# Kernel tuning notes

Measured on AMD Instinct MI355X. Metric: run time of the kernel, lower is better.

Reference implementation:

```python
import jax, jax.numpy as jnp
import numpy as np

N_NODES = 50000
N_EDGES = 800000
IN_DIM = 128
OUT_DIM = 64


def setup_inputs() -> dict:
    key = jax.random.key(0)
    k1, k2, k3, k4, k5 = jax.random.split(key, 5)
    x = jax.random.normal(k1, (N_NODES, IN_DIM), dtype=jnp.float32)
    # Glorot-uniform-ish init for the GCN weight (weight_variable_glorot)
    limit = np.sqrt(6.0 / (IN_DIM + OUT_DIM)).astype(np.float32)
    weight = jax.random.uniform(k2, (IN_DIM, OUT_DIM), dtype=jnp.float32,
                                minval=-limit, maxval=limit)
    adj_row = jax.random.randint(k3, (N_EDGES,), 0, N_NODES, dtype=jnp.int32)
    adj_col = jax.random.randint(k4, (N_EDGES,), 0, N_NODES, dtype=jnp.int32)
    adj_val = jax.random.uniform(k5, (N_EDGES,), dtype=jnp.float32)
    return {"x": x, "weight": weight, "adj_row": adj_row,
            "adj_col": adj_col, "adj_val": adj_val}


def reference(x, weight, adj_row, adj_col, adj_val):
    # x: [N, F_in], weight: [F_in, F_out]; dropout=0.0 (default) is identity.
    xw = jnp.matmul(x, weight)                      # [N, F_out] dense GEMM
    # spmm(adj, xw) with adj in COO: gather neighbor feats, scale, scatter-add
    msg = adj_val[:, None] * xw[adj_col]            # [E, F_out]
    agg = jax.ops.segment_sum(msg, adj_row, num_segments=x.shape[0])  # [N, F_out]
    return jax.nn.relu(agg)
```

## Files before the change

### kernel.cpp

```cpp
#include <hip/hip_runtime.h>

#define IN_DIM 128
#define OUT_DIM 64
#define PADK 136
#define RB 64
#define RBSH 6
#define CAPB 1280
#define AB2 128

typedef float f32x4 __attribute__((ext_vector_type(4)));
typedef short bf16x8 __attribute__((ext_vector_type(8)));

__device__ __forceinline__ unsigned short f2bf(float f) {
    unsigned u = __float_as_uint(f);
    return (unsigned short)((u + 0x7FFFu + ((u >> 16) & 1u)) >> 16);
}
__device__ __forceinline__ float bf2f(unsigned short h) {
    return __uint_as_float((unsigned)h << 16);
}

__device__ __forceinline__ void gemm_body(const float* __restrict__ x,
                                          const float* __restrict__ w,
                                          unsigned short* __restrict__ xwb,
                                          int N, int blk) {
    __shared__ unsigned short Ahi[64 * PADK];
    __shared__ unsigned short Alo[64 * PADK];
    __shared__ unsigned short Bhi[64 * PADK];
    __shared__ unsigned short Blo[64 * PADK];

    const int t = threadIdx.x;
    const int r0 = blk * 64;

    {
        const int c = t >> 2;
        const int kb = (t & 3) * 32;
        for (int k4 = 0; k4 < 32; k4 += 4) {
            ushort4 h, l;
            float v0 = w[(kb + k4 + 0) * OUT_DIM + c];
            float v1 = w[(kb + k4 + 1) * OUT_DIM + c];
            float v2 = w[(kb + k4 + 2) * OUT_DIM + c];
            float v3 = w[(kb + k4 + 3) * OUT_DIM + c];
            h.x = f2bf(v0); l.x = f2bf(v0 - bf2f(h.x));
            h.y = f2bf(v1); l.y = f2bf(v1 - bf2f(h.y));
            h.z = f2bf(v2); l.z = f2bf(v2 - bf2f(h.z));
            h.w = f2bf(v3); l.w = f2bf(v3 - bf2f(h.w));
            *(ushort4*)&Bhi[c * PADK + kb + k4] = h;
            *(ushort4*)&Blo[c * PADK + kb + k4] = l;
        }
    }
    {
        const float4* x4 = (const float4*)x;
        for (int i = 0; i < 8; ++i) {
            const int f = i * 256 + t;
            const int rr = f >> 5;
            const int kk = (f & 31) * 4;
            int row = r0 + rr; if (row >= N) row = N - 1;
            float4 v = x4[(size_t)row * (IN_DIM / 4) + (kk >> 2)];
            ushort4 h, l;
            h.x = f2bf(v.x); l.x = f2bf(v.x - bf2f(h.x));
            h.y = f2bf(v.y); l.y = f2bf(v.y - bf2f(h.y));
            h.z = f2bf(v.z); l.z = f2bf(v.z - bf2f(h.z));
            h.w = f2bf(v.w); l.w = f2bf(v.w - bf2f(h.w));
            *(ushort4*)&Ahi[rr * PADK + kk] = h;
            *(ushort4*)&Alo[rr * PADK + kk] = l;
        }
    }
    __syncthreads();

    const int lane = t & 63;
    const int wv = t >> 6;
    const int m = lane & 15;
    const int quad = lane >> 4;

    bf16x8 ahi[4], alo[4];
#pragma unroll
    for (int ks = 0; ks < 4; ++ks) {
        const int off = (wv * 16 + m) * PADK + ks * 32 + quad * 8;
        ahi[ks] = *(const bf16x8*)&Ahi[off];
        alo[ks] = *(const bf16x8*)&Alo[off];
    }
#pragma unroll
    for (int ct = 0; ct < 4; ++ct) {
        f32x4 acc = {0.f, 0.f, 0.f, 0.f};
#pragma unroll
        for (int ks = 0; ks < 4; ++ks) {
            const int off = (ct * 16 + m) * PADK + ks * 32 + quad * 8;
            bf16x8 bh = *(const bf16x8*)&Bhi[off];
            bf16x8 bl = *(const bf16x8*)&Blo[off];
            acc = __builtin_amdgcn_mfma_f32_16x16x32_bf16(alo[ks], bh, acc, 0, 0, 0);
            acc = __builtin_amdgcn_mfma_f32_16x16x32_bf16(ahi[ks], bl, acc, 0, 0, 0);
            acc = __builtin_amdgcn_mfma_f32_16x16x32_bf16(ahi[ks], bh, acc, 0, 0, 0);
        }
#pragma unroll
        for (int i = 0; i < 4; ++i) {
            const int row = r0 + wv * 16 + quad * 4 + i;
            if (row < N) xwb[(size_t)row * OUT_DIM + ct * 16 + m] = f2bf(acc[i]);
        }
    }
}

__global__ __launch_bounds__(256) void gemm_only(const float* __restrict__ x,
                                                 const float* __restrict__ w,
                                                 unsigned short* __restrict__ xwb,
                                                 int N) {
    gemm_body(x, w, xwb, N, blockIdx.x);
}

__global__ __launch_bounds__(256) void afill(
        const int* __restrict__ arow, const int* __restrict__ acol,
        const float* __restrict__ aval, int* __restrict__ pcur,
        int* __restrict__ ocount, uint4* __restrict__ olist,
        uint2* __restrict__ payload, int E, int NB, int chunk) {
    __shared__ int cnt[1024];
    __shared__ int base[1024];
    const int t = threadIdx.x;
    const int lo = blockIdx.x * chunk;
    const int hi = min(E, lo + chunk);
    if (lo >= hi) return;
    for (int i = t; i < NB; i += 256) cnt[i] = 0;
    __syncthreads();
    for (int e = lo + t; e < hi; e += 256)
        atomicAdd(&cnt[arow[e] >> RBSH], 1);
    __syncthreads();
    for (int i = t; i < NB; i += 256) {
        const int c = cnt[i];
        base[i] = c ? atomicAdd(&pcur[i], c) : 0;
        cnt[i] = 0;
    }
    __syncthreads();
    for (int e = lo + t; e < hi; e += 256) {
        const int r = arow[e];
        const int b = r >> RBSH;
        const int slot = base[b] + atomicAdd(&cnt[b], 1);
        const unsigned w0 = (unsigned)acol[e] | ((unsigned)(r & (RB - 1)) << 16);
        const unsigned w1 = __float_as_uint(aval[e]);
        if (slot < CAPB) {
            payload[(size_t)b * CAPB + slot] = make_uint2(w0, w1);
        } else {
            const int oi = atomicAdd(ocount, 1);
            olist[oi] = make_uint4((unsigned)r, (unsigned)acol[e], w1, 0u);
        }
    }
}

__global__ __launch_bounds__(512) void bagg3(
        const int* __restrict__ pcur, const uint2* __restrict__ payload,
        const unsigned short* __restrict__ xwb, float* __restrict__ out, int N,
        const int* __restrict__ ocount, const uint4* __restrict__ olist) {
    __shared__ uint2 stage[CAPB];
    __shared__ int bins[RB + 1];
    __shared__ int pl[RB];
    const int t = threadIdx.x;
    const int lane = t & 63;
    const int wv = t >> 6;
    const int b = blockIdx.x;
    const int r0 = b << RBSH;

    const int cnt = min(pcur[b], CAPB);
    if (t <= RB) bins[t] = 0;
    if (t < RB) pl[t] = 0;
    __syncthreads();

    const uint2* pay = payload + (size_t)b * CAPB;
    for (int i = t; i < cnt; i += 512)
        atomicAdd(&bins[(pay[i].x >> 16) & (RB - 1)], 1);
    __syncthreads();
    if (t == 0) {
        int run = 0;
        for (int i = 0; i < RB; ++i) { int v = bins[i]; bins[i] = run; run += v; }
        bins[RB] = run;
    }
    __syncthreads();
    for (int i = t; i < cnt; i += 512) {
        const uint2 e = pay[i];
        const int rl = (e.x >> 16) & (RB - 1);
        stage[bins[rl] + atomicAdd(&pl[rl], 1)] = e;
    }
    __syncthreads();

    float acc[8];
#pragma unroll
    for (int lr = 0; lr < 8; ++lr) {
        const int row = wv * 8 + lr;
        int j = bins[row];
        const int end = bins[row + 1];
        float a = 0.f;
        for (; j + 4 <= end; j += 4) {
            uint2 e0 = stage[j], e1 = stage[j+1], e2 = stage[j+2], e3 = stage[j+3];
            float g0 = bf2f(xwb[(size_t)(e0.x & 0xFFFF) * OUT_DIM + lane]);
            float g1 = bf2f(xwb[(size_t)(e1.x & 0xFFFF) * OUT_DIM + lane]);
            float g2 = bf2f(xwb[(size_t)(e2.x & 0xFFFF) * OUT_DIM + lane]);
            float g3 = bf2f(xwb[(size_t)(e3.x & 0xFFFF) * OUT_DIM + lane]);
            a = fmaf(__uint_as_float(e0.y), g0, a);
            a = fmaf(__uint_as_float(e1.y), g1, a);
            a = fmaf(__uint_as_float(e2.y), g2, a);
            a = fmaf(__uint_as_float(e3.y), g3, a);
        }
        for (; j < end; ++j) {
            uint2 e0 = stage[j];
            a = fmaf(__uint_as_float(e0.y),
                     bf2f(xwb[(size_t)(e0.x & 0xFFFF) * OUT_DIM + lane]), a);
        }
        acc[lr] = a;
    }

    const int oc = *ocount;
    for (int i = 0; i < oc; ++i) {
        const uint4 e = olist[i];
        const int lr = (int)e.x - r0 - wv * 8;
        if (lr >= 0 && lr < 8)
            acc[lr] += __uint_as_float(e.z) *
                       bf2f(xwb[(size_t)e.y * OUT_DIM + lane]);
    }

#pragma unroll
    for (int lr = 0; lr < 8; ++lr) {
        const int row = r0 + wv * 8 + lr;
        if (row < N) {
            const float v = acc[lr];
            out[(size_t)row * OUT_DIM + lane] = v > 0.f ? v : 0.f;
        }
    }
}

__global__ __launch_bounds__(256) void scatter_edges(
        const int* __restrict__ arow, const int* __restrict__ acol,
        const float* __restrict__ aval, const unsigned short* __restrict__ xwb,
        float* __restrict__ out, int E) {
    const int lane = threadIdx.x & 63;
    int gw = (blockIdx.x * 256 + (int)threadIdx.x) >> 6;
    const int nw = (gridDim.x * 256) >> 6;
    for (int e = gw; e < E; e += nw) {
        const float m = aval[e] * bf2f(xwb[(size_t)acol[e] * OUT_DIM + lane]);
        atomicAdd(&out[(size_t)arow[e] * OUT_DIM + lane], m);
    }
}

__global__ __launch_bounds__(256) void relu_inplace(float* __restrict__ o, int n4) {
    float4* p = (float4*)o;
    int i = blockIdx.x * 256 + threadIdx.x;
    const int stride = gridDim.x * 256;
    for (; i < n4; i += stride) {
        float4 v = p[i];
        v.x = v.x > 0.f ? v.x : 0.f;
        v.y = v.y > 0.f ? v.y : 0.f;
        v.z = v.z > 0.f ? v.z : 0.f;
        v.w = v.w > 0.f ? v.w : 0.f;
        p[i] = v;
    }
}

static inline size_t align256(size_t x) { return (x + 255) & ~(size_t)255; }

extern "C" void kernel_launch(void* const* d_in, const int* in_sizes, int n_in,
                              void* d_out, int out_size, void* d_ws, size_t ws_size,
                              hipStream_t stream) {
    const float* x    = (const float*)d_in[0];
    const float* w    = (const float*)d_in[1];
    const int*   arow = (const int*)d_in[2];
    const int*   acol = (const int*)d_in[3];
    const float* aval = (const float*)d_in[4];
    float*       out  = (float*)d_out;

    const int N  = in_sizes[0] / IN_DIM;
    const int E  = in_sizes[2];
    const int NB = (N + RB - 1) >> RBSH;
    const int GB = (N + 63) / 64;

    char* ws = (char*)d_ws;
    const size_t szXW  = align256((size_t)N * OUT_DIM * sizeof(unsigned short));
    const size_t szCnt = align256((size_t)(NB + 1) * sizeof(int));
    const size_t szOl  = align256((size_t)E * sizeof(uint4));
    const size_t szPay = (size_t)NB * CAPB * sizeof(uint2);
    const size_t need0 = szXW + szCnt + szOl + szPay;

    unsigned short* xwb = (unsigned short*)ws;
    int*   pcur    = (int*)(ws + szXW);
    int*   ocount  = pcur + NB;
    uint4* olist   = (uint4*)(ws + szXW + szCnt);
    uint2* payload = (uint2*)(ws + szXW + szCnt + szOl);

    if (ws_size >= need0 && N <= 65536 && NB <= 1024) {
        (void)hipMemsetAsync(pcur, 0, (size_t)(NB + 1) * sizeof(int), stream);
        gemm_only<<<GB, 256, 0, stream>>>(x, w, xwb, N);
        const int chunk = (E + AB2 - 1) / AB2;
        afill<<<AB2, 256, 0, stream>>>(arow, acol, aval, pcur, ocount, olist,
                                       payload, E, NB, chunk);
        bagg3<<<NB, 512, 0, stream>>>(pcur, payload, xwb, out, N, ocount, olist);
    } else {
        gemm_only<<<GB, 256, 0, stream>>>(x, w, xwb, N);
        (void)hipMemsetAsync(d_out, 0, (size_t)out_size * sizeof(float), stream);
        scatter_edges<<<4096, 256, 0, stream>>>(arow, acol, aval, xwb, out, E);
        relu_inplace<<<2048, 256, 0, stream>>>(out, out_size / 4);
    }
}
```

Baseline: 143.6 us.

## Merge GEMM and edge-binning into one launch; unroll gather loop with dual accumulators

The dense GEMM and the COO edge-binning (afill) kernels now run as one launch. The first AB2 blocks do binning and the rest do GEMM tiles, sharing one LDS buffer. Because the two phases are independent, they can overlap on the GPU and one launch boundary is removed. The aggregation loop is also unrolled to 8 gathers per iteration with two accumulators, giving more loads in flight and shorter FMA dependency chains. The cost is more registers, and every binning block now reserves the full GEMM-sized LDS allocation, which may reduce occupancy.

```diff
diff --git a/kernel.cpp b/kernel.cpp
--- a/kernel.cpp
+++ b/kernel.cpp
@@ -22,11 +22,12 @@
 __device__ __forceinline__ void gemm_body(const float* __restrict__ x,
                                           const float* __restrict__ w,
                                           unsigned short* __restrict__ xwb,
-                                          int N, int blk) {
-    __shared__ unsigned short Ahi[64 * PADK];
-    __shared__ unsigned short Alo[64 * PADK];
-    __shared__ unsigned short Bhi[64 * PADK];
-    __shared__ unsigned short Blo[64 * PADK];
+                                          int N, int blk,
+                                          unsigned short* lds) {
+    unsigned short* Ahi = lds;
+    unsigned short* Alo = lds + 64 * PADK;
+    unsigned short* Bhi = lds + 2 * 64 * PADK;
+    unsigned short* Blo = lds + 3 * 64 * PADK;
 
     const int t = threadIdx.x;
     const int r0 = blk * 64;
@@ -99,22 +100,16 @@
     }
 }
 
-__global__ __launch_bounds__(256) void gemm_only(const float* __restrict__ x,
-                                                 const float* __restrict__ w,
-                                                 unsigned short* __restrict__ xwb,
-                                                 int N) {
-    gemm_body(x, w, xwb, N, blockIdx.x);
-}
-
-__global__ __launch_bounds__(256) void afill(
+__device__ __forceinline__ void afill_body(
         const int* __restrict__ arow, const int* __restrict__ acol,
         const float* __restrict__ aval, int* __restrict__ pcur,
         int* __restrict__ ocount, uint4* __restrict__ olist,
-        uint2* __restrict__ payload, int E, int NB, int chunk) {
-    __shared__ int cnt[1024];
-    __shared__ int base[1024];
+        uint2* __restrict__ payload, int E, int NB, int chunk, int blk,
+        int* ldsi) {
+    int* cnt  = ldsi;
+    int* base = ldsi + 1024;
     const int t = threadIdx.x;
-    const int lo = blockIdx.x * chunk;
+    const int lo = blk * chunk;
     const int hi = min(E, lo + chunk);
     if (lo >= hi) return;
     for (int i = t; i < NB; i += 256) cnt[i] = 0;
@@ -141,6 +136,30 @@
             olist[oi] = make_uint4((unsigned)r, (unsigned)acol[e], w1, 0u);
         }
     }
+}
+
+__global__ __launch_bounds__(256) void gemm_afill(
+        const float* __restrict__ x, const float* __restrict__ w,
+        unsigned short* __restrict__ xwb, int N,
+        const int* __restrict__ arow, const int* __restrict__ acol,
+        const float* __restrict__ aval, int* __restrict__ pcur,
+        int* __restrict__ ocount, uint4* __restrict__ olist,
+        uint2* __restrict__ payload, int E, int NB, int chunk) {
+    __shared__ unsigned short LB[4 * 64 * PADK];
+    if ((int)blockIdx.x < AB2) {
+        afill_body(arow, acol, aval, pcur, ocount, olist, payload, E, NB,
+                   chunk, blockIdx.x, (int*)LB);
+    } else {
+        gemm_body(x, w, xwb, N, blockIdx.x - AB2, LB);
+    }
+}
+
+__global__ __launch_bounds__(256) void gemm_only(const float* __restrict__ x,
+                                                 const float* __restrict__ w,
+                                                 unsigned short* __restrict__ xwb,
+                                                 int N) {
+    __shared__ unsigned short LB[4 * 64 * PADK];
+    gemm_body(x, w, xwb, N, blockIdx.x, LB);
 }
 
 __global__ __launch_bounds__(512) void bagg3(
@@ -184,24 +203,44 @@
         const int row = wv * 8 + lr;
         int j = bins[row];
         const int end = bins[row + 1];
-        float a = 0.f;
+        float a0 = 0.f, a1 = 0.f;
+        for (; j + 8 <= end; j += 8) {
+            uint2 e0 = stage[j],   e1 = stage[j+1], e2 = stage[j+2], e3 = stage[j+3];
+            uint2 e4 = stage[j+4], e5 = stage[j+5], e6 = stage[j+6], e7 = stage[j+7];
+            float g0 = bf2f(xwb[(size_t)(e0.x & 0xFFFF) * OUT_DIM + lane]);
+            float g1 = bf2f(xwb[(size_t)(e1.x & 0xFFFF) * OUT_DIM + lane]);
+            float g2 = bf2f(xwb[(size_t)(e2.x & 0xFFFF) * OUT_DIM + lane]);
+            float g3 = bf2f(xwb[(size_t)(e3.x & 0xFFFF) * OUT_DIM + lane]);
+            float g4 = bf2f(xwb[(size_t)(e4.x & 0xFFFF) * OUT_DIM + lane]);
+            float g5 = bf2f(xwb[(size_t)(e5.x & 0xFFFF) * OUT_DIM + lane]);
+            float g6 = bf2f(xwb[(size_t)(e6.x & 0xFFFF) * OUT_DIM + lane]);
+            float g7 = bf2f(xwb[(size_t)(e7.x & 0xFFFF) * OUT_DIM + lane]);
+            a0 = fmaf(__uint_as_float(e0.y), g0, a0);
+            a1 = fmaf(__uint_as_float(e1.y), g1, a1);
+            a0 = fmaf(__uint_as_float(e2.y), g2, a0);
+            a1 = fmaf(__uint_as_float(e3.y), g3, a1);
+            a0 = fmaf(__uint_as_float(e4.y), g4, a0);
+            a1 = fmaf(__uint_as_float(e5.y), g5, a1);
+            a0 = fmaf(__uint_as_float(e6.y), g6, a0);
+            a1 = fmaf(__uint_as_float(e7.y), g7, a1);
+        }
         for (; j + 4 <= end; j += 4) {
             uint2 e0 = stage[j], e1 = stage[j+1], e2 = stage[j+2], e3 = stage[j+3];
             float g0 = bf2f(xwb[(size_t)(e0.x & 0xFFFF) * OUT_DIM + lane]);
             float g1 = bf2f(xwb[(size_t)(e1.x & 0xFFFF) * OUT_DIM + lane]);
             float g2 = bf2f(xwb[(size_t)(e2.x & 0xFFFF) * OUT_DIM + lane]);
             float g3 = bf2f(xwb[(size_t)(e3.x & 0xFFFF) * OUT_DIM + lane]);
-            a = fmaf(__uint_as_float(e0.y), g0, a);
-            a = fmaf(__uint_as_float(e1.y), g1, a);
-            a = fmaf(__uint_as_float(e2.y), g2, a);
-            a = fmaf(__uint_as_float(e3.y), g3, a);
+            a0 = fmaf(__uint_as_float(e0.y), g0, a0);
+            a1 = fmaf(__uint_as_float(e1.y), g1, a1);
+            a0 = fmaf(__uint_as_float(e2.y), g2, a0);
+            a1 = fmaf(__uint_as_float(e3.y), g3, a1);
         }
         for (; j < end; ++j) {
             uint2 e0 = stage[j];
-            a = fmaf(__uint_as_float(e0.y),
-                     bf2f(xwb[(size_t)(e0.x & 0xFFFF) * OUT_DIM + lane]), a);
-        }
-        acc[lr] = a;
+            a0 = fmaf(__uint_as_float(e0.y),
+                      bf2f(xwb[(size_t)(e0.x & 0xFFFF) * OUT_DIM + lane]), a0);
+        }
+        acc[lr] = a0 + a1;
     }
 
     const int oc = *ocount;
@@ -282,10 +321,10 @@
 
     if (ws_size >= need0 && N <= 65536 && NB <= 1024) {
         (void)hipMemsetAsync(pcur, 0, (size_t)(NB + 1) * sizeof(int), stream);
-        gemm_only<<<GB, 256, 0, stream>>>(x, w, xwb, N);
         const int chunk = (E + AB2 - 1) / AB2;
-        afill<<<AB2, 256, 0, stream>>>(arow, acol, aval, pcur, ocount, olist,
-                                       payload, E, NB, chunk);
+        gemm_afill<<<AB2 + GB, 256, 0, stream>>>(x, w, xwb, N, arow, acol, aval,
+                                                 pcur, ocount, olist, payload,
+                                                 E, NB, chunk);
         bagg3<<<NB, 512, 0, stream>>>(pcur, payload, xwb, out, N, ocount, olist);
     } else {
         gemm_only<<<GB, 256, 0, stream>>>(x, w, xwb, N);
```

Result: faster. 131.8 us (-8.2%).
